# Kernel optimization log

Hardware: AMD Instinct MI355X
Metric: run time of the kernel (lower is better)

## Reference

```python
import jax, jax.numpy as jnp
import numpy as np

IN_C, HID1, HID2 = 128, 256, 32
N_NODES = 50000
N_EDGES = 1600000
N_LABEL = 200000


def setup_inputs() -> dict:
    key = jax.random.key(0)
    ks = jax.random.split(key, 8)
    x = jax.random.normal(ks[0], (N_NODES, IN_C), dtype=jnp.float32)
    edge_index = jax.random.randint(ks[1], (2, N_EDGES), 0, N_NODES, dtype=jnp.int64)
    edge_label_index = jax.random.randint(ks[2], (2, N_LABEL), 0, N_NODES, dtype=jnp.int64)
    # GCNConv params (glorot-ish scale), bias zeros as default init
    W1 = jax.random.normal(ks[3], (IN_C, HID1), dtype=jnp.float32) * (1.0 / np.sqrt(IN_C))
    b1 = jnp.zeros((HID1,), dtype=jnp.float32)
    W2 = jax.random.normal(ks[4], (HID1, HID2), dtype=jnp.float32) * (1.0 / np.sqrt(HID1))
    b2 = jnp.zeros((HID2,), dtype=jnp.float32)
    return {"x": x, "edge_index": edge_index, "edge_label_index": edge_label_index,
            "W1": W1, "b1": b1, "W2": W2, "b2": b2}


def _gcn_conv(x, W, b, src, dst, n_nodes):
    # GCNConv: h = x @ W; add self-loops; symmetric deg^{-1/2} normalization; scatter-add; + bias
    h = x @ W  # [N, out]
    loop = jnp.arange(n_nodes, dtype=src.dtype)
    s = jnp.concatenate([src, loop])
    d = jnp.concatenate([dst, loop])
    deg = jax.ops.segment_sum(jnp.ones_like(d, dtype=h.dtype), d, num_segments=n_nodes)
    dinv = jnp.where(deg > 0, jax.lax.rsqrt(deg), 0.0)
    coef = dinv[s] * dinv[d]  # [E+N]
    msg = h[s] * coef[:, None]  # irregular gather, [E+N, out]
    agg = jax.ops.segment_sum(msg, d, num_segments=n_nodes)
    return agg + b


def reference(x, edge_index, edge_label_index, W1, b1, W2, b2):
    n = x.shape[0]
    src, dst = edge_index[0], edge_index[1]
    # encode (dropout p=0, use_bn=False -> identity)
    h = _gcn_conv(x, W1, b1, src, dst, n)
    h = jax.nn.relu(h)
    z = _gcn_conv(h, W2, b2, src, dst, n)
    # decode: edge-wise dot product
    return (z[edge_label_index[0]] * z[edge_label_index[1]]).sum(axis=-1)
```

## Files before the change

### kernel.cpp

```cpp
#include <hip/hip_runtime.h>
#include <hip/hip_fp16.h>

#define IN_C 128
#define H1   256
#define H2   32
#define BWL  6
#define NBMAX 1024
#define BCAP 2560
#define CSRCAP 4096

typedef _Float16 half8 __attribute__((ext_vector_type(8)));
typedef _Float16 half4 __attribute__((ext_vector_type(4)));
typedef _Float16 h2    __attribute__((ext_vector_type(2)));
typedef float f32x4 __attribute__((ext_vector_type(4)));
typedef unsigned short us8 __attribute__((ext_vector_type(8)));
typedef unsigned short us4 __attribute__((ext_vector_type(4)));

__global__ __launch_bounds__(256) void k_scatter(const int* __restrict__ src, const int* __restrict__ dst,
                                                 int* bucket_cursor, unsigned int* __restrict__ binned,
                                                 const float* __restrict__ W1, const float* __restrict__ W2,
                                                 _Float16* __restrict__ W1s, _Float16* __restrict__ W2s,
                                                 int e, int nb) {
  __shared__ int hist[NBMAX];
  __shared__ int wbase[NBMAX];
  int t = threadIdx.x;
  for (int u = t; u < nb; u += 256) hist[u] = 0;
  __syncthreads();
  int base = blockIdx.x * 8192;
  int s_[32], d_[32], r_[32];
  #pragma unroll
  for (int j = 0; j < 32; j++) {
    int i = base + j * 256 + t;
    if (i < e) {
      s_[j] = src[i]; d_[j] = dst[i];
      r_[j] = atomicAdd(&hist[d_[j] >> BWL], 1);
    } else d_[j] = -1;
  }
  __syncthreads();
  for (int u = t; u < nb; u += 256) {
    int c = hist[u];
    wbase[u] = (c > 0) ? (u * BCAP + atomicAdd(&bucket_cursor[u], c)) : 0;
  }
  __syncthreads();
  #pragma unroll
  for (int j = 0; j < 32; j++) {
    if (d_[j] >= 0)
      binned[wbase[d_[j] >> BWL] + r_[j]] = ((unsigned)(d_[j] & 63) << 16) | (unsigned)s_[j];
  }
  int i = blockIdx.x * 256 + t;
  if (i < 128 * 256) {
    int d = i >> 3, j = i & 7;
    int mrow = d & 15, quad = (d >> 4) & 3, ks = (d >> 6) & 3, nt = d >> 8;
    W1s[i] = (_Float16)W1[(ks * 32 + quad * 8 + j) * 256 + nt * 16 + mrow];
  }
  if (i < 32 * 256) {
    int d = i >> 3, j = i & 7;
    int mrow = d & 15, quad = (d >> 4) & 3, ks = (d >> 6) & 7, nt = d >> 9;
    W2s[i] = (_Float16)W2[(ks * 32 + quad * 8 + j) * 32 + nt * 16 + mrow];
  }
}

__global__ __launch_bounds__(256) void k_fill2(const unsigned int* __restrict__ binned,
                                               const int* __restrict__ bucket_cursor,
                                               unsigned short* __restrict__ csr16,
                                               int* __restrict__ offsets, int* __restrict__ ecnt,
                                               float* __restrict__ dinv,
                                               const float4* __restrict__ x4, half4* __restrict__ xh4,
                                               int n, int nb) {
  __shared__ int cnt[64], pre[64], loc[64];
  __shared__ float sdinv[64];
  int b = blockIdx.x;
  int t = threadIdx.x;
  if (t < 64) cnt[t] = 0;
  {
    us8 dv;
    #pragma unroll
    for (int q = 0; q < 8; q++) dv[q] = (unsigned short)n;
    us8* cp = (us8*)(csr16 + (size_t)b * CSRCAP);
    for (int i = t; i < CSRCAP / 8; i += 256) cp[i] = dv;
  }
  __syncthreads();
  int start = b * BCAP, end = start + bucket_cursor[b];
  int startc = b * CSRCAP;
  int node0 = b << BWL;
  unsigned int recs[10]; int ranks[10];
  int ne = 0;
  for (int i = start + t; i < end; i += 256) {
    unsigned int rec = binned[i];
    int li = (int)(rec >> 16);
    ranks[ne] = atomicAdd(&cnt[li], 1);
    recs[ne++] = rec;
  }
  __syncthreads();
  int v = (t < 64) ? cnt[t] : 0;
  int vp = (v + 31) & ~31;
  if (t < 64) pre[t] = vp;
  __syncthreads();
  for (int off = 1; off < 64; off <<= 1) {
    int x = (t >= off && t < 64) ? pre[t - off] : 0;
    __syncthreads();
    if (t < 64) pre[t] += x;
    __syncthreads();
  }
  if (t < 64) {
    int excl = pre[t] - vp;
    loc[t] = excl;
    float dn = rsqrtf((float)(v + 1));
    sdinv[t] = dn;
    int node = node0 + t;
    if (node < n) {
      offsets[node] = startc + excl;
      ecnt[node] = v;
      dinv[node] = dn;
    }
  }
  __syncthreads();
  for (int k = 0; k < ne; k++) {
    int li = (int)(recs[k] >> 16);
    csr16[startc + loc[li] + ranks[k]] = (unsigned short)(recs[k] & 0xFFFFu);
  }
  for (int q = t; q < 64 * 32; q += 256) {
    int nd = node0 + (q >> 5);
    if (nd < n) {
      int c4 = q & 31;
      float4 vv = x4[(size_t)nd * 32 + c4];
      float dn = sdinv[q >> 5];
      half4 o;
      o[0] = (_Float16)(vv.x * dn); o[1] = (_Float16)(vv.y * dn);
      o[2] = (_Float16)(vv.z * dn); o[3] = (_Float16)(vv.w * dn);
      xh4[(size_t)nd * 32 + c4] = o;
    }
  }
}

__global__ __launch_bounds__(256, 2) void k_agg1(const half8* __restrict__ xh8, const float* __restrict__ dinv,
                                                 const int* __restrict__ ecnt, const int* __restrict__ offsets,
                                                 const unsigned short* __restrict__ csr16,
                                                 half8* __restrict__ aggh8, int n) {
  int node = blockIdx.x * 4 + (threadIdx.x >> 6);
  int lane = threadIdx.x & 63;
  int g = lane >> 4;
  int c8 = lane & 15;
  if (node >= n) return;
  float acc[8];
  #pragma unroll
  for (int k = 0; k < 8; k++) acc[k] = 0.f;
  int start = offsets[node];
  int cnt = ecnt[node];
  int nche = (cnt + 31) & ~31;
  int j = 0;
  for (; j + 64 <= nche; j += 64) {
    us8 i0 = *(const us8*)(csr16 + start + j + g * 8);
    us8 i1 = *(const us8*)(csr16 + start + j + 32 + g * 8);
    half8 v0 = xh8[(size_t)i0[0] * 16 + c8],  v1 = xh8[(size_t)i0[1] * 16 + c8];
    half8 v2 = xh8[(size_t)i0[2] * 16 + c8],  v3 = xh8[(size_t)i0[3] * 16 + c8];
    half8 v4 = xh8[(size_t)i0[4] * 16 + c8],  v5 = xh8[(size_t)i0[5] * 16 + c8];
    half8 v6 = xh8[(size_t)i0[6] * 16 + c8],  v7 = xh8[(size_t)i0[7] * 16 + c8];
    half8 w0 = xh8[(size_t)i1[0] * 16 + c8],  w1 = xh8[(size_t)i1[1] * 16 + c8];
    half8 w2 = xh8[(size_t)i1[2] * 16 + c8],  w3 = xh8[(size_t)i1[3] * 16 + c8];
    half8 w4 = xh8[(size_t)i1[4] * 16 + c8],  w5 = xh8[(size_t)i1[5] * 16 + c8];
    half8 w6 = xh8[(size_t)i1[6] * 16 + c8],  w7 = xh8[(size_t)i1[7] * 16 + c8];
    half8 sA = (((v0 + v1) + (v2 + v3)) + ((v4 + v5) + (v6 + v7)));
    half8 sB = (((w0 + w1) + (w2 + w3)) + ((w4 + w5) + (w6 + w7)));
    #pragma unroll
    for (int k = 0; k < 8; k++) { acc[k] += (float)sA[k]; acc[k] += (float)sB[k]; }
  }
  if (j < nche) {
    us8 i0 = *(const us8*)(csr16 + start + j + g * 8);
    half8 v0 = xh8[(size_t)i0[0] * 16 + c8],  v1 = xh8[(size_t)i0[1] * 16 + c8];
    half8 v2 = xh8[(size_t)i0[2] * 16 + c8],  v3 = xh8[(size_t)i0[3] * 16 + c8];
    half8 v4 = xh8[(size_t)i0[4] * 16 + c8],  v5 = xh8[(size_t)i0[5] * 16 + c8];
    half8 v6 = xh8[(size_t)i0[6] * 16 + c8],  v7 = xh8[(size_t)i0[7] * 16 + c8];
    half8 s = (((v0 + v1) + (v2 + v3)) + ((v4 + v5) + (v6 + v7)));
    #pragma unroll
    for (int k = 0; k < 8; k++) acc[k] += (float)s[k];
  }
  #pragma unroll
  for (int k = 0; k < 8; k++) {
    acc[k] += __shfl_xor(acc[k], 16, 64);
    acc[k] += __shfl_xor(acc[k], 32, 64);
  }
  if (g == 0) {
    half8 selfv = xh8[(size_t)node * 16 + c8];
    float dn = dinv[node];
    half8 o;
    #pragma unroll
    for (int k = 0; k < 8; k++) o[k] = (_Float16)((acc[k] + (float)selfv[k]) * dn);
    aggh8[(size_t)node * 16 + c8] = o;
  }
}

__global__ __launch_bounds__(256) void k_gemm12(const _Float16* __restrict__ aggh,
                                                const _Float16* __restrict__ W1s, const float* __restrict__ b1,
                                                const _Float16* __restrict__ W2s, const float* __restrict__ dinv,
                                                _Float16* __restrict__ h2h, int n) {
  __shared__ _Float16 wlds[128 * 256];
  int wid = threadIdx.x >> 6, lane = threadIdx.x & 63;
  int quad = lane >> 4, mrow = lane & 15;
  int mbase = blockIdx.x * 64 + wid * 16;
  int node = mbase + mrow; if (node >= n) node = n - 1;
  {
    half8* wl8 = (half8*)wlds;
    const half8* wg8 = (const half8*)W1s;
    for (int i = threadIdx.x; i < 4096; i += 256) wl8[i] = wg8[i];
  }
  __syncthreads();
  const half8* A = (const half8*)aggh;
  const half8* BL = (const half8*)wlds;
  f32x4 acc[16];
  #pragma unroll
  for (int t = 0; t < 16; t++) acc[t] = (f32x4){0.f, 0.f, 0.f, 0.f};
  half8 a_cur = A[(size_t)node * 16 + quad];
  #pragma unroll
  for (int ks = 0; ks < 4; ks++) {
    half8 a = a_cur;
    if (ks < 3) a_cur = A[(size_t)node * 16 + (ks + 1) * 4 + quad];
    #pragma unroll
    for (int nt = 0; nt < 16; nt++) {
      half8 b = BL[(nt * 4 + ks) * 64 + lane];
      acc[nt] = __builtin_amdgcn_mfma_f32_16x16x32_f16(a, b, acc[nt], 0, 0, 0);
    }
  }
  __syncthreads();
  _Float16* h1t = wlds;
  #pragma unroll
  for (int nt = 0; nt < 16; nt++) {
    int c = nt * 16 + mrow;
    float bias = b1[c];
    #pragma unroll
    for (int r = 0; r < 4; r++)
      h1t[(wid * 16 + quad * 4 + r) * 264 + c] = (_Float16)fmaxf(acc[nt][r] + bias, 0.f);
  }
  __syncthreads();
  const half8* B2 = (const half8*)W2s;
  f32x4 acc2[2];
  acc2[0] = (f32x4){0.f, 0.f, 0.f, 0.f};
  acc2[1] = (f32x4){0.f, 0.f, 0.f, 0.f};
  #pragma unroll
  for (int ks = 0; ks < 8; ks++) {
    const half8* arow = (const half8*)&h1t[(wid * 16 + mrow) * 264 + ks * 32 + quad * 8];
    half8 a = *arow;
    half8 b0 = B2[(0 * 8 + ks) * 64 + lane];
    half8 b1f = B2[(1 * 8 + ks) * 64 + lane];
    acc2[0] = __builtin_amdgcn_mfma_f32_16x16x32_f16(a, b0,  acc2[0], 0, 0, 0);
    acc2[1] = __builtin_amdgcn_mfma_f32_16x16x32_f16(a, b1f, acc2[1], 0, 0, 0);
  }
  #pragma unroll
  for (int nt = 0; nt < 2; nt++) {
    int c = nt * 16 + mrow;
    #pragma unroll
    for (int r = 0; r < 4; r++) {
      int m = mbase + quad * 4 + r;
      if (m < n) h2h[(size_t)m * H2 + c] = (_Float16)(acc2[nt][r] * dinv[m]);
    }
  }
}

__global__ __launch_bounds__(256, 2) void k_agg2(const half4* __restrict__ h2h4, const float* __restrict__ dinv,
                                                 const int* __restrict__ ecnt, const int* __restrict__ offsets,
                                                 const unsigned short* __restrict__ csr16,
                                                 const float* __restrict__ b2, half4* __restrict__ zh4, int n) {
  int node = blockIdx.x * 4 + (threadIdx.x >> 6);
  int lane = threadIdx.x & 63;
  int g = lane >> 3;
  int c4 = lane & 7;
  if (node >= n) return;
  float acc[4];
  #pragma unroll
  for (int k = 0; k < 4; k++) acc[k] = 0.f;
  int start = offsets[node];
  int cnt = ecnt[node];
  int nche = (cnt + 31) & ~31;
  int j = 0;
  for (; j + 64 <= nche; j += 64) {
    us4 i0 = *(const us4*)(csr16 + start + j + g * 4);
    us4 i1 = *(const us4*)(csr16 + start + j + 32 + g * 4);
    half4 vA = h2h4[(size_t)i0[0] * 8 + c4], vB = h2h4[(size_t)i0[1] * 8 + c4];
    half4 vC = h2h4[(size_t)i0[2] * 8 + c4], vD = h2h4[(size_t)i0[3] * 8 + c4];
    half4 vE = h2h4[(size_t)i1[0] * 8 + c4], vF = h2h4[(size_t)i1[1] * 8 + c4];
    half4 vG = h2h4[(size_t)i1[2] * 8 + c4], vH = h2h4[(size_t)i1[3] * 8 + c4];
    half4 t1 = (vA + vB) + (vC + vD);
    half4 t2 = (vE + vF) + (vG + vH);
    #pragma unroll
    for (int k = 0; k < 4; k++) { acc[k] += (float)t1[k]; acc[k] += (float)t2[k]; }
  }
  if (j < nche) {
    us4 i0 = *(const us4*)(csr16 + start + j + g * 4);
    half4 vA = h2h4[(size_t)i0[0] * 8 + c4], vB = h2h4[(size_t)i0[1] * 8 + c4];
    half4 vC = h2h4[(size_t)i0[2] * 8 + c4], vD = h2h4[(size_t)i0[3] * 8 + c4];
    half4 s = (vA + vB) + (vC + vD);
    #pragma unroll
    for (int k = 0; k < 4; k++) acc[k] += (float)s[k];
  }
  #pragma unroll
  for (int k = 0; k < 4; k++) {
    acc[k] += __shfl_xor(acc[k], 8, 64);
    acc[k] += __shfl_xor(acc[k], 16, 64);
    acc[k] += __shfl_xor(acc[k], 32, 64);
  }
  if (g == 0) {
    half4 selfv = h2h4[(size_t)node * 8 + c4];
    float dn = dinv[node];
    half4 o;
    #pragma unroll
    for (int k = 0; k < 4; k++) o[k] = (_Float16)((acc[k] + (float)selfv[k]) * dn + b2[c4 * 4 + k]);
    zh4[(size_t)node * 8 + c4] = o;
  }
}

__global__ __launch_bounds__(512) void k_decode(const half4* __restrict__ zh4, const int* __restrict__ eli,
                                                float* __restrict__ out, int L) {
  int p = blockIdx.x * 64 + (threadIdx.x >> 3);
  int c4 = threadIdx.x & 7;
  if (p >= L) return;
  int a = eli[p], b = eli[L + p];
  half4 za = zh4[(size_t)a * 8 + c4];
  half4 zb = zh4[(size_t)b * 8 + c4];
  h2 zal = {za[0], za[1]}, zah = {za[2], za[3]};
  h2 zbl = {zb[0], zb[1]}, zbh = {zb[2], zb[3]};
  float v = __builtin_amdgcn_fdot2(zal, zbl, __builtin_amdgcn_fdot2(zah, zbh, 0.f, false), false);
  #pragma unroll
  for (int off = 4; off >= 1; off >>= 1) v += __shfl_xor(v, off, 64);
  if (c4 == 0) out[p] = v;
}

extern "C" void kernel_launch(void* const* d_in, const int* in_sizes, int n_in,
                              void* d_out, int out_size, void* d_ws, size_t ws_size,
                              hipStream_t stream) {
  const float* x   = (const float*)d_in[0];
  const int*   ei  = (const int*)d_in[1];
  const int*   eli = (const int*)d_in[2];
  const float* W1  = (const float*)d_in[3];
  const float* b1  = (const float*)d_in[4];
  const float* W2  = (const float*)d_in[5];
  const float* b2  = (const float*)d_in[6];
  float* out = (float*)d_out;

  const int N = in_sizes[0] / IN_C;
  const int E = in_sizes[1] / 2;
  const int L = in_sizes[2] / 2;
  const int* e_src = ei;
  const int* e_dst = ei + E;
  const int NB = (N + 63) >> BWL;

  char* p = (char*)d_ws;
  auto carve = [&](size_t bytes) -> void* {
    void* r = (void*)p;
    p += (bytes + 255) & ~(size_t)255;
    return r;
  };
  int*   ecnt      = (int*)  carve((size_t)N * 4);
  float* dinv      = (float*)carve((size_t)N * 4);
  int*   offsets   = (int*)  carve((size_t)N * 4);
  int*   bcursor   = (int*)  carve((NBMAX + 1) * 4);
  _Float16* W1s    = (_Float16*)carve(256 * 128 * 2);
  _Float16* W2s    = (_Float16*)carve(32 * 256 * 2);
  unsigned short* csr16 = (unsigned short*)carve((size_t)NB * CSRCAP * 2);
  unsigned int* binned  = (unsigned int*)carve((size_t)NB * BCAP * 4);
  h2*    xh        = (h2*)   carve((size_t)(N + 1) * IN_C * 2);
  h2*    aggh      = (h2*)   carve(((size_t)N + 64) * IN_C * 2);
  _Float16* h2h    = (_Float16*)carve(((size_t)N + 64) * H2 * 2);
  half4* zh4       = (half4*)carve((size_t)N * H2 * 2);
  half4* h2h4 = (half4*)h2h;

  const int B = 256;
  hipMemsetAsync(bcursor, 0, (size_t)(NBMAX + 1) * 4, stream);
  hipMemsetAsync((char*)xh + (size_t)N * IN_C * 2, 0, IN_C * 2, stream);
  hipMemsetAsync((char*)h2h + (size_t)N * H2 * 2, 0, H2 * 2, stream);
  k_scatter<<<(E + 8191) / 8192, B, 0, stream>>>(e_src, e_dst, bcursor, binned,
                                                 W1, W2, W1s, W2s, E, NB);
  k_fill2<<<NB, B, 0, stream>>>(binned, bcursor, csr16, offsets, ecnt, dinv,
                                (const float4*)x, (half4*)xh, N, NB);
  k_agg1<<<(N + 3) / 4, B, 0, stream>>>((const half8*)xh, dinv, ecnt, offsets, csr16, (half8*)aggh, N);
  k_gemm12<<<(N + 63) / 64, B, 0, stream>>>((const _Float16*)aggh, W1s, b1, W2s, dinv, h2h, N);
  k_agg2<<<(N + 3) / 4, B, 0, stream>>>(h2h4, dinv, ecnt, offsets, csr16, b2, zh4, N);
  k_decode<<<(L + 63) / 64, 512, 0, stream>>>(zh4, eli, out, L);
}
```

Baseline: 219.4 us.

## Split layer-1 aggregation into four column passes and software-pipeline CSR index loads

```diff
diff --git a/kernel.cpp b/kernel.cpp
--- a/kernel.cpp
+++ b/kernel.cpp
@@ -14,7 +14,6 @@
 typedef _Float16 h2    __attribute__((ext_vector_type(2)));
 typedef float f32x4 __attribute__((ext_vector_type(4)));
 typedef unsigned short us8 __attribute__((ext_vector_type(8)));
-typedef unsigned short us4 __attribute__((ext_vector_type(4)));
 
 __global__ __launch_bounds__(256) void k_scatter(const int* __restrict__ src, const int* __restrict__ dst,
                                                  int* bucket_cursor, unsigned int* __restrict__ binned,
@@ -133,50 +132,41 @@
   }
 }
 
-__global__ __launch_bounds__(256, 2) void k_agg1(const half8* __restrict__ xh8, const float* __restrict__ dinv,
-                                                 const int* __restrict__ ecnt, const int* __restrict__ offsets,
-                                                 const unsigned short* __restrict__ csr16,
-                                                 half8* __restrict__ aggh8, int n) {
-  int node = blockIdx.x * 4 + (threadIdx.x >> 6);
+__global__ __launch_bounds__(256) void k_agg1(const half8* __restrict__ xh8, const float* __restrict__ dinv,
+                                              const int* __restrict__ ecnt, const int* __restrict__ offsets,
+                                              const unsigned short* __restrict__ csr16,
+                                              half8* __restrict__ aggh8, int n, int nblk) {
+  int pass = blockIdx.x / nblk;
+  int blk  = blockIdx.x - pass * nblk;
+  int node = blk * 4 + (threadIdx.x >> 6);
   int lane = threadIdx.x & 63;
-  int g = lane >> 4;
-  int c8 = lane & 15;
+  int g  = lane >> 2;
+  int c8 = (lane & 3) + pass * 4;
   if (node >= n) return;
   float acc[8];
   #pragma unroll
   for (int k = 0; k < 8; k++) acc[k] = 0.f;
   int start = offsets[node];
   int cnt = ecnt[node];
-  int nche = (cnt + 31) & ~31;
-  int j = 0;
-  for (; j + 64 <= nche; j += 64) {
-    us8 i0 = *(const us8*)(csr16 + start + j + g * 8);
-    us8 i1 = *(const us8*)(csr16 + start + j + 32 + g * 8);
-    half8 v0 = xh8[(size_t)i0[0] * 16 + c8],  v1 = xh8[(size_t)i0[1] * 16 + c8];
-    half8 v2 = xh8[(size_t)i0[2] * 16 + c8],  v3 = xh8[(size_t)i0[3] * 16 + c8];
-    half8 v4 = xh8[(size_t)i0[4] * 16 + c8],  v5 = xh8[(size_t)i0[5] * 16 + c8];
-    half8 v6 = xh8[(size_t)i0[6] * 16 + c8],  v7 = xh8[(size_t)i0[7] * 16 + c8];
-    half8 w0 = xh8[(size_t)i1[0] * 16 + c8],  w1 = xh8[(size_t)i1[1] * 16 + c8];
-    half8 w2 = xh8[(size_t)i1[2] * 16 + c8],  w3 = xh8[(size_t)i1[3] * 16 + c8];
-    half8 w4 = xh8[(size_t)i1[4] * 16 + c8],  w5 = xh8[(size_t)i1[5] * 16 + c8];
-    half8 w6 = xh8[(size_t)i1[6] * 16 + c8],  w7 = xh8[(size_t)i1[7] * 16 + c8];
-    half8 sA = (((v0 + v1) + (v2 + v3)) + ((v4 + v5) + (v6 + v7)));
-    half8 sB = (((w0 + w1) + (w2 + w3)) + ((w4 + w5) + (w6 + w7)));
-    #pragma unroll
-    for (int k = 0; k < 8; k++) { acc[k] += (float)sA[k]; acc[k] += (float)sB[k]; }
-  }
-  if (j < nche) {
-    us8 i0 = *(const us8*)(csr16 + start + j + g * 8);
-    half8 v0 = xh8[(size_t)i0[0] * 16 + c8],  v1 = xh8[(size_t)i0[1] * 16 + c8];
-    half8 v2 = xh8[(size_t)i0[2] * 16 + c8],  v3 = xh8[(size_t)i0[3] * 16 + c8];
-    half8 v4 = xh8[(size_t)i0[4] * 16 + c8],  v5 = xh8[(size_t)i0[5] * 16 + c8];
-    half8 v6 = xh8[(size_t)i0[6] * 16 + c8],  v7 = xh8[(size_t)i0[7] * 16 + c8];
-    half8 s = (((v0 + v1) + (v2 + v3)) + ((v4 + v5) + (v6 + v7)));
-    #pragma unroll
-    for (int k = 0; k < 8; k++) acc[k] += (float)s[k];
+  int units = ((cnt + 31) & ~31) >> 5;
+  int s0 = csr16[start + g], s1 = csr16[start + 16 + g];
+  for (int u = 0; u < units; u++) {
+    int t0 = 0, t1 = 0;
+    if (u + 1 < units) {
+      int nb = start + ((u + 1) << 5) + g;
+      t0 = csr16[nb]; t1 = csr16[nb + 16];
+    }
+    half8 v0 = xh8[(size_t)s0 * 16 + c8];
+    half8 v1 = xh8[(size_t)s1 * 16 + c8];
+    half8 sA = v0 + v1;
+    #pragma unroll
+    for (int k = 0; k < 8; k++) acc[k] += (float)sA[k];
+    s0 = t0; s1 = t1;
   }
   #pragma unroll
   for (int k = 0; k < 8; k++) {
+    acc[k] += __shfl_xor(acc[k], 4, 64);
+    acc[k] += __shfl_xor(acc[k], 8, 64);
     acc[k] += __shfl_xor(acc[k], 16, 64);
     acc[k] += __shfl_xor(acc[k], 32, 64);
   }
@@ -256,10 +246,10 @@
   }
 }
 
-__global__ __launch_bounds__(256, 2) void k_agg2(const half4* __restrict__ h2h4, const float* __restrict__ dinv,
-                                                 const int* __restrict__ ecnt, const int* __restrict__ offsets,
-                                                 const unsigned short* __restrict__ csr16,
-                                                 const float* __restrict__ b2, half4* __restrict__ zh4, int n) {
+__global__ __launch_bounds__(256) void k_agg2(const half4* __restrict__ h2h4, const float* __restrict__ dinv,
+                                              const int* __restrict__ ecnt, const int* __restrict__ offsets,
+                                              const unsigned short* __restrict__ csr16,
+                                              const float* __restrict__ b2, half4* __restrict__ zh4, int n) {
   int node = blockIdx.x * 4 + (threadIdx.x >> 6);
   int lane = threadIdx.x & 63;
   int g = lane >> 3;
@@ -270,27 +260,21 @@
   for (int k = 0; k < 4; k++) acc[k] = 0.f;
   int start = offsets[node];
   int cnt = ecnt[node];
-  int nche = (cnt + 31) & ~31;
-  int j = 0;
-  for (; j + 64 <= nche; j += 64) {
-    us4 i0 = *(const us4*)(csr16 + start + j + g * 4);
-    us4 i1 = *(const us4*)(csr16 + start + j + 32 + g * 4);
-    half4 vA = h2h4[(size_t)i0[0] * 8 + c4], vB = h2h4[(size_t)i0[1] * 8 + c4];
-    half4 vC = h2h4[(size_t)i0[2] * 8 + c4], vD = h2h4[(size_t)i0[3] * 8 + c4];
-    half4 vE = h2h4[(size_t)i1[0] * 8 + c4], vF = h2h4[(size_t)i1[1] * 8 + c4];
-    half4 vG = h2h4[(size_t)i1[2] * 8 + c4], vH = h2h4[(size_t)i1[3] * 8 + c4];
-    half4 t1 = (vA + vB) + (vC + vD);
-    half4 t2 = (vE + vF) + (vG + vH);
-    #pragma unroll
-    for (int k = 0; k < 4; k++) { acc[k] += (float)t1[k]; acc[k] += (float)t2[k]; }
-  }
-  if (j < nche) {
-    us4 i0 = *(const us4*)(csr16 + start + j + g * 4);
-    half4 vA = h2h4[(size_t)i0[0] * 8 + c4], vB = h2h4[(size_t)i0[1] * 8 + c4];
-    half4 vC = h2h4[(size_t)i0[2] * 8 + c4], vD = h2h4[(size_t)i0[3] * 8 + c4];
-    half4 s = (vA + vB) + (vC + vD);
-    #pragma unroll
-    for (int k = 0; k < 4; k++) acc[k] += (float)s[k];
+  int units = ((cnt + 31) & ~31) >> 5;
+  int s0 = csr16[start + g],      s1 = csr16[start + 8 + g];
+  int s2 = csr16[start + 16 + g], s3 = csr16[start + 24 + g];
+  for (int u = 0; u < units; u++) {
+    int t0 = 0, t1 = 0, t2 = 0, t3 = 0;
+    if (u + 1 < units) {
+      int nb = start + ((u + 1) << 5) + g;
+      t0 = csr16[nb]; t1 = csr16[nb + 8]; t2 = csr16[nb + 16]; t3 = csr16[nb + 24];
+    }
+    half4 vA = h2h4[(size_t)s0 * 8 + c4], vB = h2h4[(size_t)s1 * 8 + c4];
+    half4 vC = h2h4[(size_t)s2 * 8 + c4], vD = h2h4[(size_t)s3 * 8 + c4];
+    half4 sS = (vA + vB) + (vC + vD);
+    #pragma unroll
+    for (int k = 0; k < 4; k++) acc[k] += (float)sS[k];
+    s0 = t0; s1 = t1; s2 = t2; s3 = t3;
   }
   #pragma unroll
   for (int k = 0; k < 4; k++) {
@@ -355,7 +339,7 @@
   int*   bcursor   = (int*)  carve((NBMAX + 1) * 4);
   _Float16* W1s    = (_Float16*)carve(256 * 128 * 2);
   _Float16* W2s    = (_Float16*)carve(32 * 256 * 2);
-  unsigned short* csr16 = (unsigned short*)carve((size_t)NB * CSRCAP * 2);
+  unsigned short* csr16 = (unsigned short*)carve(((size_t)NB * CSRCAP + 64) * 2);
   unsigned int* binned  = (unsigned int*)carve((size_t)NB * BCAP * 4);
   h2*    xh        = (h2*)   carve((size_t)(N + 1) * IN_C * 2);
   h2*    aggh      = (h2*)   carve(((size_t)N + 64) * IN_C * 2);
@@ -364,6 +348,7 @@
   half4* h2h4 = (half4*)h2h;
 
   const int B = 256;
+  const int nblk = (N + 3) / 4;
   hipMemsetAsync(bcursor, 0, (size_t)(NBMAX + 1) * 4, stream);
   hipMemsetAsync((char*)xh + (size_t)N * IN_C * 2, 0, IN_C * 2, stream);
   hipMemsetAsync((char*)h2h + (size_t)N * H2 * 2, 0, H2 * 2, stream);
@@ -371,7 +356,7 @@
                                                  W1, W2, W1s, W2s, E, NB);
   k_fill2<<<NB, B, 0, stream>>>(binned, bcursor, csr16, offsets, ecnt, dinv,
                                 (const float4*)x, (half4*)xh, N, NB);
-  k_agg1<<<(N + 3) / 4, B, 0, stream>>>((const half8*)xh, dinv, ecnt, offsets, csr16, (half8*)aggh, N);
+  k_agg1<<<4 * nblk, B, 0, stream>>>((const half8*)xh, dinv, ecnt, offsets, csr16, (half8*)aggh, N, nblk);
   k_gemm12<<<(N + 63) / 64, B, 0, stream>>>((const _Float16*)aggh, W1s, b1, W2s, dinv, h2h, N);
   k_agg2<<<(N + 3) / 4, B, 0, stream>>>(h2h4, dinv, ecnt, offsets, csr16, b2, zh4, N);
   k_decode<<<(L + 63) / 64, 512, 0, stream>>>(zh4, eli, out, L);
```

Result: slower. 265.2 us (+20.9%).
